# Optimization experiments

Hardware: AMD Instinct MI355X
Metric: run time of the kernel (lower is better)

Reference implementation:

```python
import jax, jax.numpy as jnp
import numpy as np

NUM_HEADS = 16
ROPE_BASE = 10000.0


def _rope_cos_sin(seq_len, head_dim, dtype):
    inv_freq = 1.0 / (ROPE_BASE ** (jnp.arange(0, head_dim, 2, dtype=jnp.float32) / head_dim))
    t = jnp.arange(seq_len, dtype=jnp.float32)
    freqs = t[:, None] * inv_freq[None, :]          # [S, hd/2]
    emb = jnp.concatenate([freqs, freqs], axis=-1)  # [S, hd]
    return jnp.cos(emb).astype(dtype), jnp.sin(emb).astype(dtype)


def _rotate_half(x):
    x1, x2 = jnp.split(x, 2, axis=-1)
    return jnp.concatenate([-x2, x1], axis=-1)


def setup_inputs() -> dict:
    key = jax.random.key(0)
    ks = jax.random.split(key, 5)
    B, S, D = 2, 2048, 2048
    x = jax.random.normal(ks[0], (B, S, D), dtype=jnp.float32)
    Wq = jax.random.normal(ks[1], (D, D), dtype=jnp.float32) * (D ** -0.5)
    Wk = jax.random.normal(ks[2], (D, D), dtype=jnp.float32) * (D ** -0.5)
    Wv = jax.random.normal(ks[3], (D, D), dtype=jnp.float32) * (D ** -0.5)
    Wo = jax.random.normal(ks[4], (D, D), dtype=jnp.float32) * (D ** -0.5)
    return {"x": x, "Wq": Wq, "Wk": Wk, "Wv": Wv, "Wo": Wo}


def reference(x, Wq, Wk, Wv, Wo):
    B, S, D = x.shape
    H = NUM_HEADS
    hd = D // H
    scale = hd ** -0.5
    # Linear(bias=False): y = x @ W.T ; reshape to [B, H, S, hd]
    def proj(W):
        return jnp.einsum('bsd,ed->bse', x, W).reshape(B, S, H, hd).transpose(0, 2, 1, 3)
    q, k, v = proj(Wq), proj(Wk), proj(Wv)
    cos, sin = _rope_cos_sin(S, hd, x.dtype)  # [S, hd]
    cos = cos[None, None, :, :]
    sin = sin[None, None, :, :]
    q = q * cos + _rotate_half(q) * sin
    k = k * cos + _rotate_half(k) * sin
    scores = jnp.einsum('bhqd,bhkd->bhqk', q, k) * scale  # [B,H,S,S]
    causal = jnp.triu(jnp.ones((S, S), dtype=bool), k=1)
    scores = jnp.where(causal[None, None], jnp.finfo(scores.dtype).min, scores)
    attn = jax.nn.softmax(scores, axis=-1)
    out = jnp.einsum('bhqk,bhkd->bhqd', attn, v)  # [B,H,S,hd]
    out = out.transpose(0, 2, 1, 3).reshape(B, S, D)
    return jnp.einsum('bsd,ed->bse', out, Wo)
```

## Files before the change

### kernel.cpp

```cpp
#include <hip/hip_runtime.h>
#include <hip/hip_bf16.h>
#include <math.h>

typedef __bf16 bf16_t;
typedef __attribute__((ext_vector_type(8))) __bf16 bf16x8;
typedef __attribute__((ext_vector_type(4))) float f32x4;

#define S_LEN 2048
#define DM    2048
#define NH    16
#define HD    128
#define MTOT  4096

__device__ inline float finz(float v) {
    return (v == v && fabsf(v) < 1e30f) ? v : 0.f;
}

__device__ inline void gload_lds16(const bf16_t* g, bf16_t* l) {
    __builtin_amdgcn_global_load_lds(
        (const __attribute__((address_space(1))) void*)g,
        (__attribute__((address_space(3))) void*)l, 16, 0, 0);
}

__global__ __launch_bounds__(256)
void dtype_probe(const unsigned short* __restrict__ p, unsigned int* __restrict__ flag)
{
    __shared__ int tot;
    if (threadIdx.x == 0) tot = 0;
    __syncthreads();
    int weird = 0;
    for (int i = threadIdx.x; i < 4096; i += 256) {
        unsigned short u = p[2*i];
        int e = (u >> 7) & 0xFF;
        if (e >= 0xC8 || (e != 0 && e <= 0x38)) weird++;
    }
    atomicAdd(&tot, weird);
    __syncthreads();
    if (threadIdx.x == 0) *flag = (tot > 512) ? 1u : 0u;
}

__global__ __launch_bounds__(256)
void convert_in(const void* __restrict__ src, bf16_t* __restrict__ dst, int n,
                const unsigned int* __restrict__ flag)
{
    const bool f32 = (*flag != 0);
    int i = (blockIdx.x*256 + threadIdx.x)*4;
    if (i + 3 >= n) return;
    if (f32) {
        const float4 v = *(const float4*)((const float*)src + i);
        dst[i  ] = (bf16_t)v.x; dst[i+1] = (bf16_t)v.y;
        dst[i+2] = (bf16_t)v.z; dst[i+3] = (bf16_t)v.w;
    } else {
        *(uint2*)(dst + i) = *(const uint2*)((const bf16_t*)src + i);
    }
}

template<int MODE>
__global__ __launch_bounds__(256)
void gemm_bt(const bf16_t* __restrict__ A, const bf16_t* __restrict__ W,
             void* __restrict__ Cv)
{
    __shared__ bf16_t As[128*64];
    __shared__ bf16_t Ws[128*64];

    const int t    = threadIdx.x;
    const int wv   = t >> 6;
    const int lane = t & 63;
    const int c16  = lane & 15;
    const int quad = lane >> 4;
    const int wm   = wv & 1;
    const int wn   = wv >> 1;
    const int mb   = blockIdx.x;
    const int nb   = blockIdx.y;
    const int c7   = c16 & 7;

    const int srow = lane >> 3;
    const int sphy = (lane & 7) ^ srow;
    const bf16_t* Ab = A + (size_t)(mb*128 + wv*32 + srow)*DM + sphy*8;
    const bf16_t* Wb = W + (size_t)(nb*128 + wv*32 + srow)*DM + sphy*8;

    f32x4 acc[4][4];
    #pragma unroll
    for (int i = 0; i < 4; ++i)
        #pragma unroll
        for (int j = 0; j < 4; ++j)
            acc[i][j] = (f32x4){0.f, 0.f, 0.f, 0.f};

    for (int kb = 0; kb < DM/64; ++kb) {
        __syncthreads();
        #pragma unroll
        for (int i = 0; i < 4; ++i) {
            gload_lds16(Ab + (size_t)kb*64 + (size_t)i*8*DM, As + (wv*32 + i*8)*64);
            gload_lds16(Wb + (size_t)kb*64 + (size_t)i*8*DM, Ws + (wv*32 + i*8)*64);
        }
        __syncthreads();

        #pragma unroll
        for (int kk = 0; kk < 2; ++kk) {
            const int ph = ((kk*4 + quad) ^ c7) * 8;
            bf16x8 af[4], bfr[4];
            #pragma unroll
            for (int mt = 0; mt < 4; ++mt)
                af[mt] = *(const bf16x8*)(As + (wm*64 + mt*16 + c16)*64 + ph);
            #pragma unroll
            for (int nt = 0; nt < 4; ++nt)
                bfr[nt] = *(const bf16x8*)(Ws + (nt*32 + wn*16 + c16)*64 + ph);
            #pragma unroll
            for (int mt = 0; mt < 4; ++mt)
                #pragma unroll
                for (int nt = 0; nt < 4; ++nt)
                    acc[mt][nt] = __builtin_amdgcn_mfma_f32_16x16x32_bf16(
                                      af[mt], bfr[nt], acc[mt][nt], 0, 0, 0);
        }
    }

    #pragma unroll
    for (int mt = 0; mt < 4; ++mt) {
        #pragma unroll
        for (int r = 0; r < 4; ++r) {
            const int m = mb*128 + wm*64 + mt*16 + quad*4 + r;
            if (MODE == 2) {
                bf16_t* C = (bf16_t*)Cv;
                size_t base = (size_t)m*DM + nb*128;
                #pragma unroll
                for (int nt = 0; nt < 4; ++nt)
                    C[base + nt*32 + wn*16 + c16] = (bf16_t)finz(acc[mt][nt][r]);
            } else if (MODE == 3) {
                float* C = (float*)Cv;
                size_t base = (size_t)m*DM + nb*128;
                #pragma unroll
                for (int nt = 0; nt < 4; ++nt)
                    C[base + nt*32 + wn*16 + c16] = finz(acc[mt][nt][r]);
            } else {
                bf16_t* C = (bf16_t*)Cv;
                const int b = m >> 11;
                const int s = m & (S_LEN - 1);
                size_t base = ((size_t)(b*NH + nb)*S_LEN + s)*HD;
                if (MODE == 1) {
                    #pragma unroll
                    for (int nt = 0; nt < 4; ++nt)
                        C[base + nt*32 + wn*16 + c16] = (bf16_t)finz(acc[mt][nt][r]);
                } else {
                    #pragma unroll
                    for (int nt = 0; nt < 2; ++nt) {
                        int t64 = nt*32 + wn*16 + c16;
                        float invf = exp2f(-(float)t64 * 0.20762050593046014f);
                        float ang  = (float)s * invf;
                        float sn, cs;
                        sincosf(ang, &sn, &cs);
                        float lo = acc[mt][nt  ][r];
                        float hi = acc[mt][nt+2][r];
                        C[base + t64     ] = (bf16_t)finz(lo*cs - hi*sn);
                        C[base + t64 + 64] = (bf16_t)finz(hi*cs + lo*sn);
                    }
                }
            }
        }
    }
}

__global__ __launch_bounds__(256)
void transpose_v(const bf16_t* __restrict__ Vb, bf16_t* __restrict__ VT)
{
    __shared__ bf16_t Lt[64*72];
    const int t  = threadIdx.x;
    const int st = blockIdx.x;
    const int dt = blockIdx.y;
    const int bh = blockIdx.z;
    #pragma unroll
    for (int i = 0; i < 2; ++i) {
        int ch = t + i*256;
        int sr = ch >> 3, c = ch & 7;
        *(uint4*)(Lt + sr*72 + c*8) =
            *(const uint4*)(Vb + ((size_t)bh*S_LEN + st*64 + sr)*HD + dt*64 + c*8);
    }
    __syncthreads();
    #pragma unroll
    for (int i = 0; i < 2; ++i) {
        int ch = t + i*256;
        int dr = ch >> 3, c = ch & 7;
        bf16x8 v;
        #pragma unroll
        for (int j = 0; j < 8; ++j) v[j] = Lt[(c*8 + j)*72 + dr];
        *(bf16x8*)(VT + ((size_t)bh*HD + dt*64 + dr)*S_LEN + st*64 + c*8) = v;
    }
}

__global__ __launch_bounds__(256)
void flash_attn(const bf16_t* __restrict__ Q, const bf16_t* __restrict__ K,
                const bf16_t* __restrict__ VT, bf16_t* __restrict__ O)
{
    __shared__ bf16_t Ks[64*128];
    __shared__ bf16_t Vs[128*64];
    __shared__ bf16_t Ps[4*16*64];

    const int t    = threadIdx.x;
    const int wv   = t >> 6;
    const int lane = t & 63;
    const int c16  = lane & 15;
    const int quad = lane >> 4;
    const int c7   = c16 & 7;
    const int ix   = blockIdx.x;
    const int bh   = blockIdx.y;

    const float scale = 0.08838834764831845f;
    const float SMAX  = 12.0f;

    bf16x8 onesf;
    #pragma unroll
    for (int j = 0; j < 8; ++j) onesf[j] = (bf16_t)1.0f;

    for (int pass = 0; pass < 2; ++pass) {
        const int qb = pass ? ix : 31 - ix;

        bf16x8 qf[4];
        {
            const size_t qbase = ((size_t)bh*S_LEN + qb*64 + wv*16 + c16)*HD;
            #pragma unroll
            for (int kk = 0; kk < 4; ++kk)
                qf[kk] = *(const bf16x8*)(Q + qbase + kk*32 + quad*8);
        }

        f32x4 oacc[8];
        #pragma unroll
        for (int i = 0; i < 8; ++i) oacc[i] = (f32x4){0.f, 0.f, 0.f, 0.f};
        f32x4 lacc = (f32x4){0.f, 0.f, 0.f, 0.f};

        for (int kt = 0; kt <= qb; ++kt) {
            __syncthreads();
            #pragma unroll
            for (int i = 0; i < 4; ++i) {
                int rg = wv*16 + i*4 + (lane >> 4);
                int ph = (lane & 15) ^ (rg & 7);
                gload_lds16(K + ((size_t)bh*S_LEN + kt*64 + rg)*HD + ph*8,
                            Ks + (wv*16 + i*4)*128);
            }
            #pragma unroll
            for (int i = 0; i < 4; ++i) {
                int dg = wv*32 + i*8 + (lane >> 3);
                int ph = (lane & 7) ^ (dg & 7);
                gload_lds16(VT + ((size_t)bh*HD + dg)*S_LEN + kt*64 + ph*8,
                            Vs + (wv*32 + i*8)*64);
            }
            __syncthreads();

            f32x4 sacc[4];
            #pragma unroll
            for (int i = 0; i < 4; ++i) sacc[i] = (f32x4){0.f, 0.f, 0.f, 0.f};
            #pragma unroll
            for (int kk = 0; kk < 4; ++kk) {
                const int ph = ((kk*4 + quad) ^ c7) * 8;
                #pragma unroll
                for (int nt = 0; nt < 4; ++nt) {
                    bf16x8 kf = *(const bf16x8*)(Ks + (nt*16 + c16)*128 + ph);
                    sacc[nt] = __builtin_amdgcn_mfma_f32_16x16x32_bf16(
                                   qf[kk], kf, sacc[nt], 0, 0, 0);
                }
            }

            float pv[4][4];
            if (kt == qb) {
                const int q0 = qb*64 + wv*16 + quad*4;
                #pragma unroll
                for (int nt = 0; nt < 4; ++nt) {
                    const int kg = kt*64 + nt*16 + c16;
                    #pragma unroll
                    for (int r = 0; r < 4; ++r)
                        pv[nt][r] = (kg <= q0 + r)
                                  ? __expf(sacc[nt][r]*scale - SMAX) : 0.f;
                }
            } else {
                #pragma unroll
                for (int nt = 0; nt < 4; ++nt)
                    #pragma unroll
                    for (int r = 0; r < 4; ++r)
                        pv[nt][r] = __expf(sacc[nt][r]*scale - SMAX);
            }

            #pragma unroll
            for (int nt = 0; nt < 4; ++nt) {
                #pragma unroll
                for (int r = 0; r < 4; ++r) {
                    int rp = quad*4 + r;
                    int pc = (nt*2 + (c16 >> 3)) ^ (rp & 7);
                    Ps[wv*1024 + rp*64 + pc*8 + c7] = (bf16_t)pv[nt][r];
                }
            }

            #pragma unroll
            for (int ks = 0; ks < 2; ++ks) {
                const int ph = ((ks*4 + quad) ^ c7) * 8;
                bf16x8 pf = *(const bf16x8*)(Ps + wv*1024 + c16*64 + ph);
                lacc = __builtin_amdgcn_mfma_f32_16x16x32_bf16(pf, onesf, lacc, 0, 0, 0);
                #pragma unroll
                for (int dt = 0; dt < 8; ++dt) {
                    bf16x8 vf = *(const bf16x8*)(Vs + (dt*16 + c16)*64 + ph);
                    oacc[dt] = __builtin_amdgcn_mfma_f32_16x16x32_bf16(
                                   pf, vf, oacc[dt], 0, 0, 0);
                }
            }
        }

        const int b = bh >> 4, h = bh & 15;
        #pragma unroll
        for (int dt = 0; dt < 8; ++dt) {
            #pragma unroll
            for (int r = 0; r < 4; ++r) {
                const int q = qb*64 + wv*16 + quad*4 + r;
                float rl = 1.0f / fmaxf(lacc[r], 1e-37f);
                O[((size_t)(b*S_LEN + q))*DM + h*HD + dt*16 + c16] =
                    (bf16_t)finz(oacc[dt][r] * rl);
            }
        }
    }
}

extern "C" void kernel_launch(void* const* d_in, const int* in_sizes, int n_in,
                              void* d_out, int out_size, void* d_ws, size_t ws_size,
                              hipStream_t stream)
{
    const void* x_raw  = d_in[0];
    const void* Wq_raw = d_in[1];
    const void* Wk_raw = d_in[2];
    const void* Wv_raw = d_in[3];
    const void* Wo_raw = d_in[4];

    const int NX = MTOT*DM;
    const int NW = DM*DM;

    unsigned int* flag = (unsigned int*)d_ws;
    bf16_t* xb  = (bf16_t*)((char*)d_ws + 16);
    bf16_t* Wqb = xb  + NX;
    bf16_t* Wkb = Wqb + NW;
    bf16_t* Wvb = Wkb + NW;
    bf16_t* Wob = Wvb + NW;
    bf16_t* Qb  = Wob + NW;
    bf16_t* Kb  = Qb + NX;
    bf16_t* Vb  = Kb + NX;
    bf16_t* Ob  = Vb + NX;
    bf16_t* VT  = xb;

    bool out_is_f32 = true;
    {
        void* base = nullptr; size_t sz = 0;
        if (hipMemGetAddressRange((hipDeviceptr_t*)&base, &sz,
                                  (hipDeviceptr_t)d_out) == hipSuccess && sz != 0) {
            if (sz < (size_t)out_size * 3) out_is_f32 = false;
        }
    }

    dim3 bb(256);
    hipLaunchKernelGGL(dtype_probe, dim3(1), bb, 0, stream,
                       (const unsigned short*)x_raw, flag);
    hipLaunchKernelGGL(convert_in, dim3(NX/1024), bb, 0, stream, x_raw,  xb,  NX, flag);
    hipLaunchKernelGGL(convert_in, dim3(NW/1024), bb, 0, stream, Wq_raw, Wqb, NW, flag);
    hipLaunchKernelGGL(convert_in, dim3(NW/1024), bb, 0, stream, Wk_raw, Wkb, NW, flag);
    hipLaunchKernelGGL(convert_in, dim3(NW/1024), bb, 0, stream, Wv_raw, Wvb, NW, flag);
    hipLaunchKernelGGL(convert_in, dim3(NW/1024), bb, 0, stream, Wo_raw, Wob, NW, flag);

    dim3 gg(32, 16);
    hipLaunchKernelGGL((gemm_bt<0>), gg, bb, 0, stream, xb, Wqb, (void*)Qb);
    hipLaunchKernelGGL((gemm_bt<0>), gg, bb, 0, stream, xb, Wkb, (void*)Kb);
    hipLaunchKernelGGL((gemm_bt<1>), gg, bb, 0, stream, xb, Wvb, (void*)Vb);
    hipLaunchKernelGGL(transpose_v, dim3(32, 2, 32), bb, 0, stream, Vb, VT);
    hipLaunchKernelGGL(flash_attn, dim3(16, 32), bb, 0, stream, Qb, Kb, VT, Ob);
    if (out_is_f32)
        hipLaunchKernelGGL((gemm_bt<3>), gg, bb, 0, stream, Ob, Wob, d_out);
    else
        hipLaunchKernelGGL((gemm_bt<2>), gg, bb, 0, stream, Ob, Wob, d_out);
}
```

Baseline: 443.0 us.

## Switch flash attention to 32x32x16 MFMA with two waves per block

Restructures the attention kernel so each of two wavefronts owns 32 query rows and uses 32x32x16 bf16 MFMA tiles in place of four waves of 16x16x32 tiles. Q fragments, the K/V LDS fill loops, the P staging layout and swizzles, the causal mask indexing and the output write are all rewritten for the 32x32 accumulator layout. The intent is more reuse of each LDS K/V fragment per MFMA and fewer LDS reads per flop. The cost is half as many threads per block for the same 64-row tile, which lowers occupancy and latency hiding and raises register pressure from the 16-wide accumulators.

```diff
diff --git a/kernel.cpp b/kernel.cpp
--- a/kernel.cpp
+++ b/kernel.cpp
@@ -5,6 +5,7 @@
 typedef __bf16 bf16_t;
 typedef __attribute__((ext_vector_type(8))) __bf16 bf16x8;
 typedef __attribute__((ext_vector_type(4))) float f32x4;
+typedef __attribute__((ext_vector_type(16))) float f32x16;
 
 #define S_LEN 2048
 #define DM    2048
@@ -186,20 +187,19 @@
     }
 }
 
-__global__ __launch_bounds__(256)
+__global__ __launch_bounds__(128)
 void flash_attn(const bf16_t* __restrict__ Q, const bf16_t* __restrict__ K,
                 const bf16_t* __restrict__ VT, bf16_t* __restrict__ O)
 {
     __shared__ bf16_t Ks[64*128];
     __shared__ bf16_t Vs[128*64];
-    __shared__ bf16_t Ps[4*16*64];
+    __shared__ bf16_t Ps[2*32*64];
 
     const int t    = threadIdx.x;
     const int wv   = t >> 6;
     const int lane = t & 63;
-    const int c16  = lane & 15;
-    const int quad = lane >> 4;
-    const int c7   = c16 & 7;
+    const int n31  = lane & 31;
+    const int half = lane >> 5;
     const int ix   = blockIdx.x;
     const int bh   = blockIdx.y;
 
@@ -210,92 +210,105 @@
     #pragma unroll
     for (int j = 0; j < 8; ++j) onesf[j] = (bf16_t)1.0f;
 
+
     for (int pass = 0; pass < 2; ++pass) {
         const int qb = pass ? ix : 31 - ix;
 
-        bf16x8 qf[4];
+        bf16x8 qf[8];
         {
-            const size_t qbase = ((size_t)bh*S_LEN + qb*64 + wv*16 + c16)*HD;
-            #pragma unroll
-            for (int kk = 0; kk < 4; ++kk)
-                qf[kk] = *(const bf16x8*)(Q + qbase + kk*32 + quad*8);
-        }
-
-        f32x4 oacc[8];
-        #pragma unroll
-        for (int i = 0; i < 8; ++i) oacc[i] = (f32x4){0.f, 0.f, 0.f, 0.f};
-        f32x4 lacc = (f32x4){0.f, 0.f, 0.f, 0.f};
+            const size_t qbase = ((size_t)bh*S_LEN + qb*64 + wv*32 + n31)*HD;
+            #pragma unroll
+            for (int kst = 0; kst < 8; ++kst)
+                qf[kst] = *(const bf16x8*)(Q + qbase + kst*16 + half*8);
+        }
+
+        f32x16 oacc[4];
+        #pragma unroll
+        for (int i = 0; i < 4; ++i)
+            #pragma unroll
+            for (int j = 0; j < 16; ++j) oacc[i][j] = 0.f;
+        f32x16 lacc;
+        #pragma unroll
+        for (int j = 0; j < 16; ++j) lacc[j] = 0.f;
 
         for (int kt = 0; kt <= qb; ++kt) {
             __syncthreads();
             #pragma unroll
-            for (int i = 0; i < 4; ++i) {
-                int rg = wv*16 + i*4 + (lane >> 4);
+            for (int i = 0; i < 8; ++i) {
+                int rg = wv*32 + i*4 + (lane >> 4);
                 int ph = (lane & 15) ^ (rg & 7);
                 gload_lds16(K + ((size_t)bh*S_LEN + kt*64 + rg)*HD + ph*8,
-                            Ks + (wv*16 + i*4)*128);
-            }
-            #pragma unroll
-            for (int i = 0; i < 4; ++i) {
-                int dg = wv*32 + i*8 + (lane >> 3);
+                            Ks + (wv*32 + i*4)*128);
+            }
+            #pragma unroll
+            for (int i = 0; i < 8; ++i) {
+                int dg = wv*64 + i*8 + (lane >> 3);
                 int ph = (lane & 7) ^ (dg & 7);
                 gload_lds16(VT + ((size_t)bh*HD + dg)*S_LEN + kt*64 + ph*8,
-                            Vs + (wv*32 + i*8)*64);
+                            Vs + (wv*64 + i*8)*64);
             }
             __syncthreads();
 
-            f32x4 sacc[4];
-            #pragma unroll
-            for (int i = 0; i < 4; ++i) sacc[i] = (f32x4){0.f, 0.f, 0.f, 0.f};
-            #pragma unroll
-            for (int kk = 0; kk < 4; ++kk) {
-                const int ph = ((kk*4 + quad) ^ c7) * 8;
-                #pragma unroll
-                for (int nt = 0; nt < 4; ++nt) {
-                    bf16x8 kf = *(const bf16x8*)(Ks + (nt*16 + c16)*128 + ph);
-                    sacc[nt] = __builtin_amdgcn_mfma_f32_16x16x32_bf16(
-                                   qf[kk], kf, sacc[nt], 0, 0, 0);
-                }
-            }
-
-            float pv[4][4];
+            f32x16 sacc[2];
+            #pragma unroll
+            for (int i = 0; i < 2; ++i)
+                #pragma unroll
+                for (int j = 0; j < 16; ++j) sacc[i][j] = 0.f;
+            #pragma unroll
+            for (int kst = 0; kst < 8; ++kst) {
+                #pragma unroll
+                for (int nt = 0; nt < 2; ++nt) {
+                    int key = nt*32 + n31;
+                    int pc  = (kst*2 + half) ^ (key & 7);
+                    bf16x8 kf = *(const bf16x8*)(Ks + key*128 + pc*8);
+                    sacc[nt] = __builtin_amdgcn_mfma_f32_32x32x16_bf16(
+                                   qf[kst], kf, sacc[nt], 0, 0, 0);
+                }
+            }
+
+            float pv[2][16];
             if (kt == qb) {
-                const int q0 = qb*64 + wv*16 + quad*4;
-                #pragma unroll
-                for (int nt = 0; nt < 4; ++nt) {
-                    const int kg = kt*64 + nt*16 + c16;
+                const int qg0 = qb*64 + wv*32 + 4*half;
+                #pragma unroll
+                for (int nt = 0; nt < 2; ++nt) {
+                    const int kg = kt*64 + nt*32 + n31;
                     #pragma unroll
-                    for (int r = 0; r < 4; ++r)
-                        pv[nt][r] = (kg <= q0 + r)
-                                  ? __expf(sacc[nt][r]*scale - SMAX) : 0.f;
+                    for (int i = 0; i < 16; ++i) {
+                        int qg = qg0 + (i & 3) + 8*(i >> 2);
+                        pv[nt][i] = (kg <= qg)
+                                  ? __expf(sacc[nt][i]*scale - SMAX) : 0.f;
+                    }
                 }
             } else {
                 #pragma unroll
-                for (int nt = 0; nt < 4; ++nt)
+                for (int nt = 0; nt < 2; ++nt)
                     #pragma unroll
-                    for (int r = 0; r < 4; ++r)
-                        pv[nt][r] = __expf(sacc[nt][r]*scale - SMAX);
-            }
-
-            #pragma unroll
-            for (int nt = 0; nt < 4; ++nt) {
-                #pragma unroll
-                for (int r = 0; r < 4; ++r) {
-                    int rp = quad*4 + r;
-                    int pc = (nt*2 + (c16 >> 3)) ^ (rp & 7);
-                    Ps[wv*1024 + rp*64 + pc*8 + c7] = (bf16_t)pv[nt][r];
-                }
-            }
-
-            #pragma unroll
-            for (int ks = 0; ks < 2; ++ks) {
-                const int ph = ((ks*4 + quad) ^ c7) * 8;
-                bf16x8 pf = *(const bf16x8*)(Ps + wv*1024 + c16*64 + ph);
-                lacc = __builtin_amdgcn_mfma_f32_16x16x32_bf16(pf, onesf, lacc, 0, 0, 0);
-                #pragma unroll
-                for (int dt = 0; dt < 8; ++dt) {
-                    bf16x8 vf = *(const bf16x8*)(Vs + (dt*16 + c16)*64 + ph);
-                    oacc[dt] = __builtin_amdgcn_mfma_f32_16x16x32_bf16(
+                    for (int i = 0; i < 16; ++i)
+                        pv[nt][i] = __expf(sacc[nt][i]*scale - SMAX);
+            }
+
+            #pragma unroll
+            for (int nt = 0; nt < 2; ++nt) {
+                const int col = nt*32 + n31;
+                #pragma unroll
+                for (int i = 0; i < 16; ++i) {
+                    int rowf = (i & 3) + 8*(i >> 2) + 4*half;
+                    int pc   = (col >> 3) ^ (rowf & 7);
+                    Ps[wv*2048 + rowf*64 + pc*8 + (col & 7)] = (bf16_t)pv[nt][i];
+                }
+            }
+
+            #pragma unroll
+            for (int ks = 0; ks < 4; ++ks) {
+                int pcP = (ks*2 + half) ^ (n31 & 7);
+                bf16x8 pf = *(const bf16x8*)(Ps + wv*2048 + n31*64 + pcP*8);
+                lacc = __builtin_amdgcn_mfma_f32_32x32x16_bf16(pf, onesf, lacc, 0, 0, 0);
+                #pragma unroll
+                for (int dt = 0; dt < 4; ++dt) {
+                    int d  = dt*32 + n31;
+                    int pc = (ks*2 + half) ^ (d & 7);
+                    bf16x8 vf = *(const bf16x8*)(Vs + d*64 + pc*8);
+                    oacc[dt] = __builtin_amdgcn_mfma_f32_32x32x16_bf16(
                                    pf, vf, oacc[dt], 0, 0, 0);
                 }
             }
@@ -303,13 +316,13 @@
 
         const int b = bh >> 4, h = bh & 15;
         #pragma unroll
-        for (int dt = 0; dt < 8; ++dt) {
-            #pragma unroll
-            for (int r = 0; r < 4; ++r) {
-                const int q = qb*64 + wv*16 + quad*4 + r;
-                float rl = 1.0f / fmaxf(lacc[r], 1e-37f);
-                O[((size_t)(b*S_LEN + q))*DM + h*HD + dt*16 + c16] =
-                    (bf16_t)finz(oacc[dt][r] * rl);
+        for (int dt = 0; dt < 4; ++dt) {
+            #pragma unroll
+            for (int i = 0; i < 16; ++i) {
+                const int q = qb*64 + wv*32 + (i & 3) + 8*(i >> 2) + 4*half;
+                float rl = 1.0f / fmaxf(lacc[i], 1e-37f);
+                O[((size_t)(b*S_LEN + q))*DM + h*HD + dt*32 + n31] =
+                    (bf16_t)finz(oacc[dt][i] * rl);
             }
         }
     }
@@ -363,7 +376,7 @@
     hipLaunchKernelGGL((gemm_bt<0>), gg, bb, 0, stream, xb, Wkb, (void*)Kb);
     hipLaunchKernelGGL((gemm_bt<1>), gg, bb, 0, stream, xb, Wvb, (void*)Vb);
     hipLaunchKernelGGL(transpose_v, dim3(32, 2, 32), bb, 0, stream, Vb, VT);
-    hipLaunchKernelGGL(flash_attn, dim3(16, 32), bb, 0, stream, Qb, Kb, VT, Ob);
+    hipLaunchKernelGGL(flash_attn, dim3(16, 32), dim3(128), 0, stream, Qb, Kb, VT, Ob);
     if (out_is_f32)
         hipLaunchKernelGGL((gemm_bt<3>), gg, bb, 0, stream, Ob, Wob, d_out);
     else
```

New measurement: 452.8 us. 1.02x slower.
